# Optimization experiments

Measured on AMD Instinct MI355X. Metric: run time of the kernel, lower is better.

## Reference

```python
import jax, jax.numpy as jnp
import numpy as np

B, H, K, T, OUT, NH = 512, 512, 6, 60, 2, 8

def _gelu(x):
    return jax.nn.gelu(x, approximate=False)  # torch nn.GELU default = exact erf

def _layernorm(x, g, b, eps=1e-5):
    m = jnp.mean(x, axis=-1, keepdims=True)
    v = jnp.var(x, axis=-1, keepdims=True)
    return (x - m) * jax.lax.rsqrt(v + eps) * g + b

def setup_inputs() -> dict:
    key = jax.random.key(0)
    ks = iter(jax.random.split(key, 40))
    def p(shape, scale=0.02):
        return jax.random.normal(next(ks), shape, dtype=jnp.float32) * scale
    return dict(
        interaction_ctx=p((B, H), 1.0),
        cooperative_ctx=p((B, H), 1.0),
        map_ctx=p((B, H), 1.0),
        mode_queries=p((K, H)),
        # context_proj: Linear(3H,H) -> GELU -> Linear(H,H)
        Wc1=p((3 * H, H)), bc1=jnp.zeros((H,), jnp.float32),
        Wc2=p((H, H)), bc2=jnp.zeros((H,), jnp.float32),
        # coarse_heads stacked over modes: Linear(H,2H)->GELU->Linear(2H,T*OUT)
        Wk1=p((K, H, 2 * H)), bk1=jnp.zeros((K, 2 * H), jnp.float32),
        Wk2=p((K, 2 * H, T * OUT)), bk2=jnp.zeros((K, T * OUT), jnp.float32),
        # traj_encoder: Linear(OUT,H)->GELU
        Wt=p((OUT, H)), bt=jnp.zeros((H,), jnp.float32),
        # refine_attn (MultiheadAttention) projections
        Wq_a=p((H, H)), bq_a=jnp.zeros((H,), jnp.float32),
        Wk_a=p((H, H)), bk_a=jnp.zeros((H,), jnp.float32),
        Wv_a=p((H, H)), bv_a=jnp.zeros((H,), jnp.float32),
        Wo_a=p((H, H)), bo_a=jnp.zeros((H,), jnp.float32),
        ln_g=jnp.ones((H,), jnp.float32), ln_b=jnp.zeros((H,), jnp.float32),
        # refine_heads stacked over modes: Linear(H,H)->GELU->Linear(H,OUT)
        Wr1=p((K, H, H)), br1=jnp.zeros((K, H), jnp.float32),
        Wr2=p((K, H, OUT)), br2=jnp.zeros((K, OUT), jnp.float32),
        # conf_head: Linear(H,64)->ReLU->Linear(64,1)
        Wf1=p((H, 64)), bf1=jnp.zeros((64,), jnp.float32),
        Wf2=p((64, 1)), bf2=jnp.zeros((1,), jnp.float32),
    )

def reference(interaction_ctx, cooperative_ctx, map_ctx, mode_queries,
              Wc1, bc1, Wc2, bc2, Wk1, bk1, Wk2, bk2, Wt, bt,
              Wq_a, bq_a, Wk_a, bk_a, Wv_a, bv_a, Wo_a, bo_a,
              ln_g, ln_b, Wr1, br1, Wr2, br2, Wf1, bf1, Wf2, bf2):
    # dropout layers are identity in eval mode
    combined = jnp.concatenate([interaction_ctx, cooperative_ctx, map_ctx], axis=-1)  # (B,3H)
    context = _gelu(combined @ Wc1 + bc1) @ Wc2 + bc2                                 # (B,H)
    mode_features = mode_queries[None, :, :] + context[:, None, :]                    # (B,K,H)

    # coarse heads: per-mode loop -> grouped GEMM over mode axis
    h = _gelu(jnp.einsum('bkh,khf->bkf', mode_features, Wk1) + bk1)                   # (B,K,2H)
    coarse = (jnp.einsum('bkf,kfo->bko', h, Wk2) + bk2).reshape(B, K, T, OUT)          # (B,K,T,OUT)

    traj_feats = _gelu(coarse @ Wt + bt)                                              # (B,K,T,H)

    # refine_attn: keys/values are context broadcast over T (all identical), so
    # softmax weights are exactly uniform and attention output == out_proj(v_ctx).
    # (grads through Wq_a/Wk_a are exactly zero for the same reason.)
    v = context @ Wv_a + bv_a                                                         # (B,H)
    attn_out = v @ Wo_a + bo_a                                                        # (B,H)

    refined_feats = _layernorm(traj_feats + attn_out[:, None, None, :], ln_g, ln_b)   # (B,K,T,H)

    # refine heads: grouped GEMM over mode axis
    r = _gelu(jnp.einsum('bkth,khf->bktf', refined_feats, Wr1) + br1[:, None, :])     # (B,K,T,H)
    offsets = jnp.einsum('bktf,kfo->bkto', r, Wr2) + br2[:, None, :]                  # (B,K,T,OUT)
    predictions = coarse + offsets

    conf = jax.nn.relu(mode_features @ Wf1 + bf1) @ Wf2 + bf2                         # (B,K,1)
    mode_probs = jax.nn.softmax(conf[..., 0], axis=-1)                                # (B,K)
    return predictions, mode_probs
```

## Files before the change

kernel.cpp:

```cpp
#include <hip/hip_runtime.h>
#include <math.h>

#define BB 512
#define HH 512
#define KK 6
#define TT 60
#define OO 2
#define H2 1024
#define TO 120
#define RFP 520
#define HSP 1032

typedef __bf16 bf16x8 __attribute__((ext_vector_type(8)));
typedef float  f32x4  __attribute__((ext_vector_type(4)));
typedef float  f32x16 __attribute__((ext_vector_type(16)));

__device__ __forceinline__ float bf2f(unsigned short u) {
    union { unsigned int i; float f; } v; v.i = ((unsigned int)u) << 16; return v.f;
}
__device__ __forceinline__ unsigned short f2bf(float f) {
    union { float f; unsigned int i; } v; v.f = f;
    unsigned int b = v.i;
    return (unsigned short)((b + 0x7FFFu + ((b >> 16) & 1u)) >> 16);
}
__device__ __forceinline__ unsigned int pack2bf(float a, float b) {
    union { __bf16 h[2]; unsigned int u; } v;
    v.h[0] = (__bf16)a; v.h[1] = (__bf16)b;
    return v.u;
}
__device__ __forceinline__ float gelu_exact(float x) {
    return 0.5f * x * (1.0f + erff(x * 0.70710678118654752f));
}

#if defined(__has_builtin)
#  if __has_builtin(__builtin_amdgcn_rcpf)
#    define FAST_RCP(x) __builtin_amdgcn_rcpf(x)
#  endif
#  if __has_builtin(__builtin_amdgcn_exp2f)
#    define FAST_EXP2(x) __builtin_amdgcn_exp2f(x)
#  endif
#endif
#ifndef FAST_RCP
#  define FAST_RCP(x) (1.0f / (x))
#endif
#ifndef FAST_EXP2
#  define FAST_EXP2(x) __expf((x) * 0.69314718056f)
#endif

__device__ __forceinline__ float gelu_cheap(float x) {
    float x2 = x * x;
    float z = x * fmaf(0.10294324f, x2, 2.3022082f);
    float e = FAST_EXP2(-z);
    return x * FAST_RCP(1.0f + e);
}

struct F8 { float v[8]; };
__device__ __forceinline__ F8 load8f(const float* p) {
    F8 r;
    float4 a = *(const float4*)p;
    float4 b = *(const float4*)(p + 4);
    r.v[0] = a.x; r.v[1] = a.y; r.v[2] = a.z; r.v[3] = a.w;
    r.v[4] = b.x; r.v[5] = b.y; r.v[6] = b.z; r.v[7] = b.w;
    return r;
}
__device__ __forceinline__ F8 load8b(const unsigned short* p) {
    ushort4 a = *(const ushort4*)p;
    ushort4 b = *(const ushort4*)(p + 4);
    F8 r;
    r.v[0] = bf2f(a.x); r.v[1] = bf2f(a.y); r.v[2] = bf2f(a.z); r.v[3] = bf2f(a.w);
    r.v[4] = bf2f(b.x); r.v[5] = bf2f(b.y); r.v[6] = bf2f(b.z); r.v[7] = bf2f(b.w);
    return r;
}

struct PKD { const float* src; unsigned short* dst; int F, N, NC, nch, steps, Z; };
struct PK8 { PKD e[8]; };

__global__ void k_pack(PK8 d) {
    int rid = blockIdx.x * 4 + (threadIdx.x >> 6);
    const int ln = threadIdx.x & 63;
    int i = 0;
    while (i < 7) {
        int tot = d.e[i].Z * d.e[i].nch * d.e[i].steps;
        if (rid < tot) break;
        rid -= tot; ++i;
    }
    const PKD e = d.e[i];
    const int per = e.nch * e.steps;
    const int z = rid / per;
    const int r = rid - z * per;
    const int nch = r / e.steps, step = r - nch * e.steps;
    const float* src = e.src + (size_t)z * e.F * e.N;
    unsigned short* dst = e.dst + ((size_t)z * per + r) * 512 + ln * 8;
    int f_base, n;
    if (e.NC == 16) { f_base = step * 32 + (ln >> 4) * 8; n = nch * 16 + (ln & 15); }
    else            { f_base = step * 16 + (ln >> 5) * 8; n = nch * 32 + (ln & 31); }
    if (n >= e.N) n = e.N - 1;
    unsigned int pk[4];
#pragma unroll
    for (int j = 0; j < 4; ++j) {
        unsigned short lo = f2bf(src[(size_t)(f_base + 2 * j) * e.N + n]);
        unsigned short hi = f2bf(src[(size_t)(f_base + 2 * j + 1) * e.N + n]);
        pk[j] = (unsigned int)lo | ((unsigned int)hi << 16);
    }
    *(uint4*)dst = make_uint4(pk[0], pk[1], pk[2], pk[3]);
}

template <bool CONCAT, bool GELU>
__launch_bounds__(256)
__global__ void k_gemm_m(const void* __restrict__ A0, const void* __restrict__ A1,
                         const void* __restrict__ A2, const unsigned short* __restrict__ BP,
                         const float* __restrict__ bias, unsigned short* __restrict__ C,
                         int Kd) {
    __shared__ __align__(16) unsigned short As[32 * RFP];
    const int tid = threadIdx.x;
    const int bm = blockIdx.x * 32;
    const int bn = blockIdx.y * 64;
    const int w = tid >> 6, ln = tid & 63;
    const int lane15 = ln & 15, quad = ln >> 4;
    const int n = bn + w * 16 + lane15;
    const int nchunks = Kd / HH;
    const int stepsTot = Kd / 32;
    const int nchB = blockIdx.y * 4 + w;

    f32x4 acc0 = {0.f, 0.f, 0.f, 0.f}, acc1 = {0.f, 0.f, 0.f, 0.f};

    for (int kc = 0; kc < nchunks; ++kc) {
        {
            int r = tid >> 3, c0 = (tid & 7) * 64;
            unsigned short* dp = As + r * RFP + c0;
            if (CONCAT) {
                const float* src = (kc == 0) ? (const float*)A0
                                 : (kc == 1) ? (const float*)A1 : (const float*)A2;
                const float* sp = src + (bm + r) * HH + c0;
                for (int c = 0; c < 64; c += 8) {
                    F8 v = load8f(sp + c);
                    unsigned int pk[4];
#pragma unroll
                    for (int j = 0; j < 4; ++j)
                        pk[j] = pack2bf(v.v[2 * j], v.v[2 * j + 1]);
                    *(uint4*)(dp + c) = make_uint4(pk[0], pk[1], pk[2], pk[3]);
                }
            } else {
                const unsigned short* sp = (const unsigned short*)A0 + (bm + r) * HH + c0;
                for (int c = 0; c < 64; c += 8)
                    *(uint4*)(dp + c) = *(const uint4*)(sp + c);
            }
        }
        __syncthreads();
        const unsigned short* bp = BP + ((size_t)nchB * stepsTot + kc * 16) * 512 + ln * 8;
#pragma unroll
        for (int f0 = 0; f0 < HH; f0 += 32) {
            bf16x8 a0 = *(const bf16x8*)(As + lane15 * RFP + f0 + quad * 8);
            bf16x8 a1 = *(const bf16x8*)(As + (16 + lane15) * RFP + f0 + quad * 8);
            bf16x8 bf = *(const bf16x8*)(bp);
            bp += 512;
            acc0 = __builtin_amdgcn_mfma_f32_16x16x32_bf16(a0, bf, acc0, 0, 0, 0);
            acc1 = __builtin_amdgcn_mfma_f32_16x16x32_bf16(a1, bf, acc1, 0, 0, 0);
        }
        __syncthreads();
    }
    const float bb = bias[n];
#pragma unroll
    for (int reg = 0; reg < 4; ++reg) {
        float v0 = acc0[reg] + bb, v1 = acc1[reg] + bb;
        if (GELU) { v0 = gelu_exact(v0); v1 = gelu_exact(v1); }
        C[(bm + quad * 4 + reg) * HH + n] = f2bf(v0);
        C[(bm + 16 + quad * 4 + reg) * HH + n] = f2bf(v1);
    }
}

__launch_bounds__(512)
__global__ void k_bc(const unsigned short* __restrict__ ctx, const float* __restrict__ mq,
                     const unsigned short* __restrict__ Wk1P, const float* __restrict__ bk1,
                     const unsigned short* __restrict__ Wk2P, const float* __restrict__ bk2,
                     const unsigned short* __restrict__ Wf1P, const float* __restrict__ bf1,
                     const float* __restrict__ Wf2, const float* __restrict__ bf2v,
                     unsigned short* __restrict__ coarse_out, float* __restrict__ conf_out)
{
    __shared__ __align__(16) unsigned short mf[16 * RFP];
    __shared__ __align__(16) unsigned short hs[16 * HSP];

    const int tid = threadIdx.x;
    const int k = blockIdx.x % KK;
    const int b0 = (blockIdx.x / KK) * 16;
    const int w = tid >> 6;
    const int ln = tid & 63;
    const int lane15 = ln & 15;
    const int quad = ln >> 4;

    {
        int r = tid >> 5;
        int c0 = (tid & 31) * 16;
        const unsigned short* cp = ctx + (b0 + r) * HH + c0;
        const float* qp = mq + k * HH + c0;
        unsigned short* dp = mf + r * RFP + c0;
        for (int c = 0; c < 16; c += 8) {
            F8 cv = load8b(cp + c);
            F8 qv = load8f(qp + c);
            unsigned int pk[4];
#pragma unroll
            for (int j = 0; j < 4; ++j)
                pk[j] = pack2bf(cv.v[2 * j] + qv.v[2 * j], cv.v[2 * j + 1] + qv.v[2 * j + 1]);
            *(uint4*)(dp + c) = make_uint4(pk[0], pk[1], pk[2], pk[3]);
        }
    }
    __syncthreads();

    {
        const unsigned short* wk1p = Wk1P + (size_t)k * (64 * 16 * 512);
        const float* bk1p = bk1 + k * H2;
        for (int g = 0; g < 8; ++g) {
            const int n = w * 128 + g * 16 + lane15;
            f32x4 acc0 = {0.f,0.f,0.f,0.f};
            const unsigned short* bp = wk1p + (size_t)((w * 8 + g) * 16) * 512 + ln * 8;
#pragma unroll
            for (int f0 = 0; f0 < HH; f0 += 32) {
                bf16x8 a0 = *(const bf16x8*)(mf + lane15 * RFP + f0 + quad * 8);
                bf16x8 bf = *(const bf16x8*)(bp);
                bp += 512;
                acc0 = __builtin_amdgcn_mfma_f32_16x16x32_bf16(a0, bf, acc0, 0, 0, 0);
            }
            const float bias = bk1p[n];
#pragma unroll
            for (int reg = 0; reg < 4; ++reg)
                hs[(quad * 4 + reg) * HSP + n] = f2bf(gelu_exact(acc0[reg] + bias));
        }
    }
    __syncthreads();

    {
        const unsigned short* wk2p = Wk2P + (size_t)k * (8 * 32 * 512);
        const int n = w * 16 + lane15;
        f32x4 acc0 = {0.f,0.f,0.f,0.f};
        const unsigned short* bp = wk2p + (size_t)(w * 32) * 512 + ln * 8;
#pragma unroll
        for (int f0 = 0; f0 < H2; f0 += 32) {
            bf16x8 a0 = *(const bf16x8*)(hs + lane15 * HSP + f0 + quad * 8);
            bf16x8 bf = *(const bf16x8*)(bp);
            bp += 512;
            acc0 = __builtin_amdgcn_mfma_f32_16x16x32_bf16(a0, bf, acc0, 0, 0, 0);
        }
        if (n < TO) {
            const float bias = bk2[k * TO + n];
#pragma unroll
            for (int reg = 0; reg < 4; ++reg)
                coarse_out[((b0 + quad * 4 + reg) * KK + k) * TO + n] = f2bf(acc0[reg] + bias);
        }
    }

    if (w == 0) {
        f32x4 acc[4];
#pragma unroll
        for (int nt = 0; nt < 4; ++nt) { f32x4 z = {0.f,0.f,0.f,0.f}; acc[nt] = z; }
#pragma unroll
        for (int f0 = 0; f0 < HH; f0 += 32) {
            const int step = f0 >> 5;
            bf16x8 a0 = *(const bf16x8*)(mf + lane15 * RFP + f0 + quad * 8);
#pragma unroll
            for (int nt = 0; nt < 4; ++nt) {
                bf16x8 bf = *(const bf16x8*)(Wf1P + (size_t)(nt * 16 + step) * 512 + ln * 8);
                acc[nt] = __builtin_amdgcn_mfma_f32_16x16x32_bf16(a0, bf, acc[nt], 0, 0, 0);
            }
        }
        const float b2 = bf2v[0];
#pragma unroll
        for (int reg = 0; reg < 4; ++reg) {
            float s = 0.f;
#pragma unroll
            for (int nt = 0; nt < 4; ++nt) {
                const int n = nt * 16 + lane15;
                s = fmaf(fmaxf(acc[nt][reg] + bf1[n], 0.f), Wf2[n], s);
            }
#pragma unroll
            for (int off = 1; off < 16; off <<= 1) s += __shfl_xor(s, off);
            if (lane15 == 0)
                conf_out[(b0 + quad * 4 + reg) * KK + k] = s + b2;
        }
    }
}

__launch_bounds__(1024, 4)
__global__ void k_ef(
    const unsigned short* __restrict__ attn, const unsigned short* __restrict__ coarse_ws,
    const float* __restrict__ Wt,  const float* __restrict__ bt,
    const float* __restrict__ lng, const float* __restrict__ lnb,
    const unsigned short* __restrict__ Wr1P, const float* __restrict__ br1,
    const float* __restrict__ Wr2, const float* __restrict__ br2,
    float* __restrict__ pred_out)
{
    __shared__ __align__(16) unsigned short rf[2][64 * RFP];
    __shared__ float  po2[2][8][64][2];
    __shared__ float  br1d[2][HH];
    __shared__ float2 wr2d[2][HH];

    const int tid = threadIdx.x;
    const int b = blockIdx.x;
    const int w = tid >> 6;
    const int ln = tid & 63;
    const int lane31 = ln & 31;
    const int hf = ln >> 5;
    const int cbase = ln * 8;
    const int w8 = w & 7;
    const bool fwave = (w < 8);

    auto do_E = [&](int j, int buf) {
        F8 w0 = load8f(Wt + cbase);
        F8 w1 = load8f(Wt + HH + cbase);
        F8 b8 = load8f(bt + cbase);
        F8 g8 = load8f(lng + cbase);
        F8 bb8 = load8f(lnb + cbase);
        F8 a8 = load8b(attn + b * HH + cbase);
        unsigned short* rfb = &rf[buf][0];
        const unsigned short* cw = coarse_ws + (b * KK + j) * TO;
#pragma unroll
        for (int r = 0; r < 8; ++r) {
            int t = w8 + 8 * r;
            if (t < 60) {
                unsigned int cc = *(const unsigned int*)(cw + 2 * t);
                float co0 = bf2f((unsigned short)(cc & 0xffffu));
                float co1 = bf2f((unsigned short)(cc >> 16));
                float x[8]; float s = 0.f, s2 = 0.f;
#pragma unroll
                for (int jj = 0; jj < 8; ++jj) {
                    float vv = fmaf(co0, w0.v[jj], fmaf(co1, w1.v[jj], b8.v[jj]));
                    vv = gelu_cheap(vv) + a8.v[jj];
                    x[jj] = vv; s += vv; s2 = fmaf(vv, vv, s2);
                }
#pragma unroll
                for (int off = 32; off > 0; off >>= 1) {
                    s += __shfl_xor(s, off);
                    s2 += __shfl_xor(s2, off);
                }
                float mean = s * (1.0f / HH);
                float var = fmaf(-mean, mean, s2 * (1.0f / HH));
                float inv = rsqrtf(var + 1e-5f);
                unsigned int pk[4];
#pragma unroll
                for (int jj = 0; jj < 4; ++jj) {
                    float y0 = fmaf((x[2 * jj] - mean) * inv, g8.v[2 * jj], bb8.v[2 * jj]);
                    float y1 = fmaf((x[2 * jj + 1] - mean) * inv, g8.v[2 * jj + 1], bb8.v[2 * jj + 1]);
                    pk[jj] = pack2bf(y0, y1);
                }
                *(uint4*)(rfb + t * RFP + cbase) = make_uint4(pk[0], pk[1], pk[2], pk[3]);
            } else {
                *(uint4*)(rfb + t * RFP + cbase) = make_uint4(0, 0, 0, 0);
            }
        }
    };

    auto do_stage_g = [&](int j, int buf) {
        int i = tid & 511;
        br1d[buf][i] = br1[j * HH + i];
        wr2d[buf][i] = ((const float2*)Wr2)[(size_t)j * HH + i];
    };

    auto do_F = [&](int kk, int buf) {
        const unsigned short* bp0 = Wr1P + (size_t)kk * (16 * 32 * 512)
                                  + (size_t)(w8 * 2) * 32 * 512 + ln * 8;
        const unsigned short* bp1 = bp0 + 32 * 512;
        const int n0 = w8 * 64;
        const unsigned short* rfb = &rf[buf][0];
        const unsigned short* a0p = rfb + lane31 * RFP + hf * 8;
        const unsigned short* a1p = a0p + 32 * RFP;

        f32x16 acc00 = {0.f,0.f,0.f,0.f,0.f,0.f,0.f,0.f,0.f,0.f,0.f,0.f,0.f,0.f,0.f,0.f};
        f32x16 acc01 = acc00, acc10 = acc00, acc11 = acc00;

        __builtin_amdgcn_s_setprio(1);
#pragma unroll
        for (int st = 0; st < 32; ++st) {
            const int k0 = st * 16;
            bf16x8 A0 = *(const bf16x8*)(a0p + k0);
            bf16x8 A1 = *(const bf16x8*)(a1p + k0);
            bf16x8 B0 = *(const bf16x8*)(bp0 + st * 512);
            bf16x8 B1 = *(const bf16x8*)(bp1 + st * 512);
            acc00 = __builtin_amdgcn_mfma_f32_32x32x16_bf16(B0, A0, acc00, 0, 0, 0);
            acc01 = __builtin_amdgcn_mfma_f32_32x32x16_bf16(B1, A0, acc01, 0, 0, 0);
            acc10 = __builtin_amdgcn_mfma_f32_32x32x16_bf16(B0, A1, acc10, 0, 0, 0);
            acc11 = __builtin_amdgcn_mfma_f32_32x32x16_bf16(B1, A1, acc11, 0, 0, 0);
        }
        __builtin_amdgcn_s_setprio(0);

        float p00 = 0.f, p01 = 0.f, p10 = 0.f, p11 = 0.f;
#pragma unroll
        for (int nt = 0; nt < 2; ++nt) {
#pragma unroll
            for (int reg = 0; reg < 16; ++reg) {
                const int n = n0 + nt * 32 + (reg & 3) + 8 * (reg >> 2) + 4 * hf;
                const float bb = br1d[buf][n];
                const float2 w2 = wr2d[buf][n];
                const float a0v = nt ? acc01[reg] : acc00[reg];
                const float a1v = nt ? acc11[reg] : acc10[reg];
                const float rv0 = gelu_cheap(a0v + bb);
                const float rv1 = gelu_cheap(a1v + bb);
                p00 = fmaf(rv0, w2.x, p00);
                p01 = fmaf(rv0, w2.y, p01);
                p10 = fmaf(rv1, w2.x, p10);
                p11 = fmaf(rv1, w2.y, p11);
            }
        }
        p00 += __shfl_xor(p00, 32);
        p01 += __shfl_xor(p01, 32);
        p10 += __shfl_xor(p10, 32);
        p11 += __shfl_xor(p11, 32);
        if (ln < 32) {
            *(float2*)&po2[buf][w8][lane31][0]      = make_float2(p00, p01);
            *(float2*)&po2[buf][w8][32 + lane31][0] = make_float2(p10, p11);
        }
    };

    auto do_pred = [&](int kk, int buf) {
        if (tid < TO) {
            int t = tid >> 1, o = tid & 1;
            float s = 0.f;
#pragma unroll
            for (int ww = 0; ww < 8; ++ww) s += po2[buf][ww][t][o];
            float co = bf2f(coarse_ws[(b * KK + kk) * TO + tid]);
            pred_out[((b * KK + kk) * TT + t) * 2 + o] = co + s + br2[kk * 2 + o];
        }
    };

    if (!fwave) {
        do_stage_g(0, 0);
        do_E(0, 0);
    }
    __syncthreads();

    for (int kk = 0; kk < KK; ++kk) {
        const int cur = kk & 1;
        if (fwave) {
            do_F(kk, cur);
        } else if (kk < KK - 1) {
            do_stage_g(kk + 1, cur ^ 1);
            do_E(kk + 1, cur ^ 1);
        }
        __syncthreads();
        do_pred(kk, cur);
    }
}

__global__ void k_softmax(const float* __restrict__ conf, float* __restrict__ out) {
    int b = blockIdx.x * blockDim.x + threadIdx.x;
    if (b < BB) {
        float v[KK];
        float m = -1e30f;
        for (int i = 0; i < KK; ++i) { v[i] = conf[b * KK + i]; m = fmaxf(m, v[i]); }
        float s = 0.f;
        for (int i = 0; i < KK; ++i) { v[i] = __expf(v[i] - m); s += v[i]; }
        float inv = 1.0f / s;
        for (int i = 0; i < KK; ++i) out[b * KK + i] = v[i] * inv;
    }
}

extern "C" void kernel_launch(void* const* d_in, const int* in_sizes, int n_in,
                              void* d_out, int out_size, void* d_ws, size_t ws_size,
                              hipStream_t stream) {
    const float* I0  = (const float*)d_in[0];
    const float* I1  = (const float*)d_in[1];
    const float* I2  = (const float*)d_in[2];
    const float* MQ  = (const float*)d_in[3];
    const float* Wc1 = (const float*)d_in[4];
    const float* bc1 = (const float*)d_in[5];
    const float* Wc2 = (const float*)d_in[6];
    const float* bc2 = (const float*)d_in[7];
    const float* Wk1 = (const float*)d_in[8];
    const float* bk1 = (const float*)d_in[9];
    const float* Wk2 = (const float*)d_in[10];
    const float* bk2 = (const float*)d_in[11];
    const float* Wt  = (const float*)d_in[12];
    const float* bt  = (const float*)d_in[13];
    const float* Wv  = (const float*)d_in[18];
    const float* bv  = (const float*)d_in[19];
    const float* Wo  = (const float*)d_in[20];
    const float* bo  = (const float*)d_in[21];
    const float* lng = (const float*)d_in[22];
    const float* lnb = (const float*)d_in[23];
    const float* Wr1 = (const float*)d_in[24];
    const float* br1 = (const float*)d_in[25];
    const float* Wr2 = (const float*)d_in[26];
    const float* br2 = (const float*)d_in[27];
    const float* Wf1 = (const float*)d_in[28];
    const float* bf1 = (const float*)d_in[29];
    const float* Wf2 = (const float*)d_in[30];
    const float* bf2v = (const float*)d_in[31];

    unsigned short* wsu   = (unsigned short*)d_ws;
    unsigned short* wc1p  = wsu;
    unsigned short* wc2p  = wsu + 786432;
    unsigned short* wvp   = wsu + 1048576;
    unsigned short* wop   = wsu + 1310720;
    unsigned short* wk1p  = wsu + 1572864;
    unsigned short* wk2p  = wsu + 4718592;
    unsigned short* wf1p  = wsu + 5505024;
    unsigned short* wr1p  = wsu + 5537792;
    unsigned short* ctx   = wsu + 7110656;
    unsigned short* attn  = wsu + 7372800;
    unsigned short* tmp   = wsu + 7634944;
    unsigned short* coarse= wsu + 7897088;
    float* conf = (float*)(wsu + 8265728);

    float* pred = (float*)d_out;
    float* probs = pred + BB * KK * TT * OO;

    PK8 pk;
    pk.e[0] = {Wc1, wc1p, 3 * HH, HH, 16, 32, 48, 1};
    pk.e[1] = {Wc2, wc2p, HH, HH, 16, 32, 16, 1};
    pk.e[2] = {Wv,  wvp,  HH, HH, 16, 32, 16, 1};
    pk.e[3] = {Wo,  wop,  HH, HH, 16, 32, 16, 1};
    pk.e[4] = {Wk1, wk1p, HH, H2, 16, 64, 16, KK};
    pk.e[5] = {Wk2, wk2p, H2, TO, 16, 8, 32, KK};
    pk.e[6] = {Wf1, wf1p, HH, 64, 16, 4, 16, 1};
    pk.e[7] = {Wr1, wr1p, HH, HH, 32, 16, 32, KK};
    k_pack<<<dim3(3472), 256, 0, stream>>>(pk);

    k_gemm_m<true,  true ><<<dim3(16, 8), 256, 0, stream>>>(I0, I1, I2, wc1p, bc1, tmp, 3 * HH);
    k_gemm_m<false, false><<<dim3(16, 8), 256, 0, stream>>>(tmp, nullptr, nullptr, wc2p, bc2, ctx, HH);
    k_gemm_m<false, false><<<dim3(16, 8), 256, 0, stream>>>(ctx, nullptr, nullptr, wvp, bv, tmp, HH);
    k_gemm_m<false, false><<<dim3(16, 8), 256, 0, stream>>>(tmp, nullptr, nullptr, wop, bo, attn, HH);

    k_bc<<<dim3(192), 512, 0, stream>>>(ctx, MQ, wk1p, bk1, wk2p, bk2, wf1p, bf1, Wf2, bf2v,
                                        coarse, conf);
    k_ef<<<dim3(BB), 1024, 0, stream>>>(attn, coarse, Wt, bt, lng, lnb,
                                        wr1p, br1, Wr2, br2, pred);
    k_softmax<<<dim3(2), 256, 0, stream>>>(conf, probs);
}
```

Baseline: 380.8 us.

## Split refine kernel into one block per (batch, mode) without producer/consumer pipeline

The refine kernel previously ran one 1024-thread block per batch row. Half the waves built the layernormed features for the next mode while the other half ran the MFMA GEMM on the current mode, using double-buffered LDS. It now launches 512-thread blocks, one per (batch, mode) pair, that do the elementwise/layernorm stage, then the GEMM, then the reduction sequentially with single buffers. This gives six times more blocks and lower LDS per block, so the hardware can overlap work across resident blocks, in exchange for losing the explicit intra-block overlap and recomputing shared loads per mode.

```diff
diff --git a/kernel.cpp b/kernel.cpp
--- a/kernel.cpp
+++ b/kernel.cpp
@@ -279,7 +279,7 @@
     }
 }
 
-__launch_bounds__(1024, 4)
+__launch_bounds__(512, 4)
 __global__ void k_ef(
     const unsigned short* __restrict__ attn, const unsigned short* __restrict__ coarse_ws,
     const float* __restrict__ Wt,  const float* __restrict__ bt,
@@ -288,43 +288,46 @@
     const float* __restrict__ Wr2, const float* __restrict__ br2,
     float* __restrict__ pred_out)
 {
-    __shared__ __align__(16) unsigned short rf[2][64 * RFP];
-    __shared__ float  po2[2][8][64][2];
-    __shared__ float  br1d[2][HH];
-    __shared__ float2 wr2d[2][HH];
+    __shared__ __align__(16) unsigned short rf[64 * RFP];
+    __shared__ float coarse[TO];
+    __shared__ float br1s[HH];
+    __shared__ float2 wr2s[HH];
+    __shared__ float po2[8][64][2];
 
     const int tid = threadIdx.x;
-    const int b = blockIdx.x;
+    const int b = blockIdx.x / KK;
+    const int k = blockIdx.x % KK;
     const int w = tid >> 6;
     const int ln = tid & 63;
     const int lane31 = ln & 31;
     const int hf = ln >> 5;
     const int cbase = ln * 8;
-    const int w8 = w & 7;
-    const bool fwave = (w < 8);
-
-    auto do_E = [&](int j, int buf) {
+
+    const unsigned short* attb = attn + b * HH;
+
+    if (tid < TO) coarse[tid] = bf2f(coarse_ws[(b * KK + k) * TO + tid]);
+    br1s[tid] = br1[k * HH + tid];
+    wr2s[tid] = ((const float2*)Wr2)[(size_t)k * HH + tid];
+    __syncthreads();
+
+    {
         F8 w0 = load8f(Wt + cbase);
         F8 w1 = load8f(Wt + HH + cbase);
         F8 b8 = load8f(bt + cbase);
         F8 g8 = load8f(lng + cbase);
         F8 bb8 = load8f(lnb + cbase);
-        F8 a8 = load8b(attn + b * HH + cbase);
-        unsigned short* rfb = &rf[buf][0];
-        const unsigned short* cw = coarse_ws + (b * KK + j) * TO;
+        F8 a8 = load8b(attb + cbase);
 #pragma unroll
         for (int r = 0; r < 8; ++r) {
-            int t = w8 + 8 * r;
+            int t = w + 8 * r;
             if (t < 60) {
-                unsigned int cc = *(const unsigned int*)(cw + 2 * t);
-                float co0 = bf2f((unsigned short)(cc & 0xffffu));
-                float co1 = bf2f((unsigned short)(cc >> 16));
+                float co0 = coarse[2 * t], co1 = coarse[2 * t + 1];
                 float x[8]; float s = 0.f, s2 = 0.f;
 #pragma unroll
-                for (int jj = 0; jj < 8; ++jj) {
-                    float vv = fmaf(co0, w0.v[jj], fmaf(co1, w1.v[jj], b8.v[jj]));
-                    vv = gelu_cheap(vv) + a8.v[jj];
-                    x[jj] = vv; s += vv; s2 = fmaf(vv, vv, s2);
+                for (int j = 0; j < 8; ++j) {
+                    float vv = fmaf(co0, w0.v[j], fmaf(co1, w1.v[j], b8.v[j]));
+                    vv = gelu_cheap(vv) + a8.v[j];
+                    x[j] = vv; s += vv; s2 = fmaf(vv, vv, s2);
                 }
 #pragma unroll
                 for (int off = 32; off > 0; off >>= 1) {
@@ -336,31 +339,25 @@
                 float inv = rsqrtf(var + 1e-5f);
                 unsigned int pk[4];
 #pragma unroll
-                for (int jj = 0; jj < 4; ++jj) {
-                    float y0 = fmaf((x[2 * jj] - mean) * inv, g8.v[2 * jj], bb8.v[2 * jj]);
-                    float y1 = fmaf((x[2 * jj + 1] - mean) * inv, g8.v[2 * jj + 1], bb8.v[2 * jj + 1]);
-                    pk[jj] = pack2bf(y0, y1);
+                for (int j = 0; j < 4; ++j) {
+                    float y0 = fmaf((x[2 * j] - mean) * inv, g8.v[2 * j], bb8.v[2 * j]);
+                    float y1 = fmaf((x[2 * j + 1] - mean) * inv, g8.v[2 * j + 1], bb8.v[2 * j + 1]);
+                    pk[j] = pack2bf(y0, y1);
                 }
-                *(uint4*)(rfb + t * RFP + cbase) = make_uint4(pk[0], pk[1], pk[2], pk[3]);
+                *(uint4*)(rf + t * RFP + cbase) = make_uint4(pk[0], pk[1], pk[2], pk[3]);
             } else {
-                *(uint4*)(rfb + t * RFP + cbase) = make_uint4(0, 0, 0, 0);
+                *(uint4*)(rf + t * RFP + cbase) = make_uint4(0, 0, 0, 0);
             }
         }
-    };
-
-    auto do_stage_g = [&](int j, int buf) {
-        int i = tid & 511;
-        br1d[buf][i] = br1[j * HH + i];
-        wr2d[buf][i] = ((const float2*)Wr2)[(size_t)j * HH + i];
-    };
-
-    auto do_F = [&](int kk, int buf) {
-        const unsigned short* bp0 = Wr1P + (size_t)kk * (16 * 32 * 512)
-                                  + (size_t)(w8 * 2) * 32 * 512 + ln * 8;
+    }
+    __syncthreads();
+
+    {
+        const unsigned short* bp0 = Wr1P + (size_t)k * (16 * 32 * 512)
+                                  + (size_t)(w * 2) * 32 * 512 + ln * 8;
         const unsigned short* bp1 = bp0 + 32 * 512;
-        const int n0 = w8 * 64;
-        const unsigned short* rfb = &rf[buf][0];
-        const unsigned short* a0p = rfb + lane31 * RFP + hf * 8;
+        const int n0 = w * 64;
+        const unsigned short* a0p = rf + lane31 * RFP + hf * 8;
         const unsigned short* a1p = a0p + 32 * RFP;
 
         f32x16 acc00 = {0.f,0.f,0.f,0.f,0.f,0.f,0.f,0.f,0.f,0.f,0.f,0.f,0.f,0.f,0.f,0.f};
@@ -387,8 +384,8 @@
 #pragma unroll
             for (int reg = 0; reg < 16; ++reg) {
                 const int n = n0 + nt * 32 + (reg & 3) + 8 * (reg >> 2) + 4 * hf;
-                const float bb = br1d[buf][n];
-                const float2 w2 = wr2d[buf][n];
+                const float bb = br1s[n];
+                const float2 w2 = wr2s[n];
                 const float a0v = nt ? acc01[reg] : acc00[reg];
                 const float a1v = nt ? acc11[reg] : acc10[reg];
                 const float rv0 = gelu_cheap(a0v + bb);
@@ -404,38 +401,18 @@
         p10 += __shfl_xor(p10, 32);
         p11 += __shfl_xor(p11, 32);
         if (ln < 32) {
-            *(float2*)&po2[buf][w8][lane31][0]      = make_float2(p00, p01);
-            *(float2*)&po2[buf][w8][32 + lane31][0] = make_float2(p10, p11);
-        }
-    };
-
-    auto do_pred = [&](int kk, int buf) {
-        if (tid < TO) {
-            int t = tid >> 1, o = tid & 1;
-            float s = 0.f;
-#pragma unroll
-            for (int ww = 0; ww < 8; ++ww) s += po2[buf][ww][t][o];
-            float co = bf2f(coarse_ws[(b * KK + kk) * TO + tid]);
-            pred_out[((b * KK + kk) * TT + t) * 2 + o] = co + s + br2[kk * 2 + o];
-        }
-    };
-
-    if (!fwave) {
-        do_stage_g(0, 0);
-        do_E(0, 0);
+            *(float2*)&po2[w][lane31][0]      = make_float2(p00, p01);
+            *(float2*)&po2[w][32 + lane31][0] = make_float2(p10, p11);
+        }
     }
     __syncthreads();
 
-    for (int kk = 0; kk < KK; ++kk) {
-        const int cur = kk & 1;
-        if (fwave) {
-            do_F(kk, cur);
-        } else if (kk < KK - 1) {
-            do_stage_g(kk + 1, cur ^ 1);
-            do_E(kk + 1, cur ^ 1);
-        }
-        __syncthreads();
-        do_pred(kk, cur);
+    if (tid < TO) {
+        int t = tid >> 1, o = tid & 1;
+        float s = 0.f;
+#pragma unroll
+        for (int ww = 0; ww < 8; ++ww) s += po2[ww][t][o];
+        pred_out[((b * KK + k) * TT + t) * 2 + o] = coarse[tid] + s + br2[k * 2 + o];
     }
 }
 
@@ -520,7 +497,7 @@
 
     k_bc<<<dim3(192), 512, 0, stream>>>(ctx, MQ, wk1p, bk1, wk2p, bk2, wf1p, bf1, Wf2, bf2v,
                                         coarse, conf);
-    k_ef<<<dim3(BB), 1024, 0, stream>>>(attn, coarse, Wt, bt, lng, lnb,
-                                        wr1p, br1, Wr2, br2, pred);
+    k_ef<<<dim3(BB * KK), 512, 0, stream>>>(attn, coarse, Wt, bt, lng, lnb,
+                                            wr1p, br1, Wr2, br2, pred);
     k_softmax<<<dim3(2), 256, 0, stream>>>(conf, probs);
 }
```

New measurement: 330.7 us. 1.15x faster.
